# Kernel tuning notes

Measured on AMD Instinct MI355X. Metric: run time of the kernel, lower is better.

The kernel has to match this reference:

```python
import jax, jax.numpy as jnp
import numpy as np
from jax import lax

B, S = 4, 2048
HIDDEN = 1024
OUT = 1024
NUM_TABLE = 64
CODE_LEN = 10
TABLE_SIZE = 2 ** CODE_LEN  # 1024
TOTAL_DIM = NUM_TABLE * CODE_LEN  # 640


def setup_inputs() -> dict:
    key = jax.random.key(0)
    k1, k2, k3, k4, k5 = jax.random.split(key, 5)
    hidden_states = jax.random.normal(k1, (B, S, HIDDEN), dtype=jnp.float32)
    # nn.Linear(hidden_size, total_dim): weight [total_dim, hidden] in torch; store as [hidden, total_dim]
    W_proj = jax.random.normal(k2, (HIDDEN, TOTAL_DIM), dtype=jnp.float32) * (1.0 / np.sqrt(HIDDEN))
    b_proj = jax.random.normal(k3, (TOTAL_DIM,), dtype=jnp.float32) * 0.01
    tables = 0.02 * jax.random.normal(k4, (NUM_TABLE * TABLE_SIZE, OUT), dtype=jnp.float32)
    bias = 0.001 * jax.random.normal(k5, (OUT,), dtype=jnp.float32)
    return {"hidden_states": hidden_states, "W_proj": W_proj, "b_proj": b_proj,
            "tables": tables, "bias": bias}


def reference(hidden_states, W_proj, b_proj, tables, bias):
    other_shape = hidden_states.shape[:-1]
    x = hidden_states.reshape(-1, HIDDEN)  # [N, H], N = B*S
    # Hashing: dense projection then per-table code/score
    z = x @ W_proj + b_proj                       # [N, total_dim]
    z = z.reshape(-1, NUM_TABLE, CODE_LEN)        # [N, T, L]
    t = jnp.tanh(jnp.abs(z))
    score = jnp.prod((1.0 + t) * 0.5, axis=-1)    # [N, T] prob of selected bucket
    pow2 = (2 ** jnp.arange(CODE_LEN, dtype=jnp.int32))
    code = jnp.sum((z > 0).astype(jnp.int32) * pow2, axis=-1)  # [N, T] in [0, TABLE_SIZE)

    # Gather + weighted sum over tables, streamed with scan to avoid [N, T, OUT]
    tabs = tables.reshape(NUM_TABLE, TABLE_SIZE, OUT)
    code_t = code.T    # [T, N]
    score_t = score.T  # [T, N]

    def body(acc, inp):
        tab, idx, w = inp  # tab [TABLE_SIZE, OUT], idx [N], w [N]
        return acc + tab[idx] * w[:, None], None

    acc0 = jnp.zeros((x.shape[0], OUT), dtype=hidden_states.dtype)
    out, _ = lax.scan(body, acc0, (tabs, code_t, score_t))
    out = out + bias
    return out.reshape(*other_shape, OUT)
```

## Files before the change

### kernel.cpp

```cpp
#include <hip/hip_runtime.h>
#include <cstddef>
#include <cstdint>

#define HIDDEN    1024
#define OUTD      1024
#define NUM_TABLE 64
#define CODE_LEN  10
#define TABLE_SZ  1024
#define TOTAL_DIM 640

#define TAU   1e-3f
#define FCAP  131072u

typedef float  fx4    __attribute__((ext_vector_type(4)));
typedef ushort ux4    __attribute__((ext_vector_type(4)));
typedef ushort ux8    __attribute__((ext_vector_type(8)));
typedef short  bf16x8 __attribute__((ext_vector_type(8)));
typedef float  f32x4  __attribute__((ext_vector_type(4)));

struct bfp { ushort hi, lo; };
static __device__ __forceinline__ bfp split2(float v) {
    uint32_t u  = __float_as_uint(v);
    float    fh = __uint_as_float(u & 0xFFFF0000u);
    uint32_t ul = __float_as_uint(v - fh);
    bfp r; r.hi = (ushort)(u >> 16); r.lo = (ushort)(ul >> 16);
    return r;
}
static __device__ __forceinline__ ushort f2bf(float f) {
    uint32_t u = __float_as_uint(f);
    return (ushort)((u + 0x7FFFu + ((u >> 16) & 1u)) >> 16);
}

__global__ __launch_bounds__(256)
void split_wt(const float* __restrict__ W, ushort* __restrict__ wht,
              ushort* __restrict__ wlt, float* __restrict__ wt32)
{
    __shared__ float t[32][33];
    const int d0 = blockIdx.x * 32, k0 = blockIdx.y * 32;
    const int lx = threadIdx.x & 31, ly = threadIdx.x >> 5;
    #pragma unroll
    for (int i = 0; i < 32; i += 8)
        t[ly + i][lx] = W[(size_t)(k0 + ly + i) * TOTAL_DIM + d0 + lx];
    __syncthreads();
    #pragma unroll
    for (int i = 0; i < 32; i += 8) {
        float v = t[lx][ly + i];
        bfp s = split2(v);
        size_t o = (size_t)(d0 + ly + i) * HIDDEN + k0 + lx;
        wht[o] = s.hi; wlt[o] = s.lo; wt32[o] = v;
    }
}

#define GBM 64
#define GBN 64
#define GBK 32
#define LDK 40
#define GEMM_MB (8192 / GBM)
#define GEMM_NB (TOTAL_DIM / GBN)
#define GEMM_BLKS (GEMM_MB * GEMM_NB)
#define CONV_BLKS 1024

__global__ __launch_bounds__(256)
void gemm_convert(const float* __restrict__ x, const ushort* __restrict__ wht,
                  const ushort* __restrict__ wlt, const float* __restrict__ bproj,
                  float* __restrict__ z,
                  const float* __restrict__ tables, ushort* __restrict__ btab)
{
    __shared__ ushort Ah[GBM][LDK];
    __shared__ ushort Al[GBM][LDK];
    __shared__ ushort Bh[GBN][LDK];
    __shared__ ushort Bl[GBN][LDK];

    const int gb  = blockIdx.x;
    const int tid = threadIdx.x;

    if (gb >= GEMM_BLKS) {
        const int cb = gb - GEMM_BLKS;
        const int n4 = NUM_TABLE * TABLE_SZ * (OUTD / 4);
        const fx4* tp = (const fx4*)tables;
        const int stride = CONV_BLKS * 256;
        for (int i = cb * 256 + tid; i < n4; i += stride) {
            fx4 v = __builtin_nontemporal_load(&tp[i]);
            ux4 u;
            u.x = f2bf(v.x); u.y = f2bf(v.y); u.z = f2bf(v.z); u.w = f2bf(v.w);
            *(ux4*)&btab[(size_t)i * 4] = u;
        }
        return;
    }

    const int lane = tid & 63, wid = tid >> 6;
    const int wr = wid >> 1, wc = wid & 1;
    const int brow = (gb % GEMM_MB) * GBM;
    const int bcol = (gb / GEMM_MB) * GBN;
    const int fr = lane & 15, fq = lane >> 4;

    f32x4 acc[2][2] = {};

    for (int k0 = 0; k0 < HIDDEN; k0 += GBK) {
        #pragma unroll
        for (int i = 0; i < 2; ++i) {
            int c = tid + i * 256;
            int r = c >> 3, kc = (c & 7) * 4;
            fx4 v = *(const fx4*)&x[(size_t)(brow + r) * HIDDEN + k0 + kc];
            bfp s0 = split2(v.x), s1 = split2(v.y), s2 = split2(v.z), s3 = split2(v.w);
            ux4 h, l;
            h.x = s0.hi; l.x = s0.lo;
            h.y = s1.hi; l.y = s1.lo;
            h.z = s2.hi; l.z = s2.lo;
            h.w = s3.hi; l.w = s3.lo;
            *(ux4*)&Ah[r][kc] = h;
            *(ux4*)&Al[r][kc] = l;
        }
        {
            int nr = tid >> 2, kc = (tid & 3) * 8;
            size_t o = (size_t)(bcol + nr) * HIDDEN + k0 + kc;
            *(ux8*)&Bh[nr][kc] = *(const ux8*)&wht[o];
            *(ux8*)&Bl[nr][kc] = *(const ux8*)&wlt[o];
        }
        __syncthreads();

        bf16x8 ah[2], al[2], bh[2], bl[2];
        #pragma unroll
        for (int m = 0; m < 2; ++m) {
            ah[m] = *(const bf16x8*)&Ah[wr * 32 + m * 16 + fr][fq * 8];
            al[m] = *(const bf16x8*)&Al[wr * 32 + m * 16 + fr][fq * 8];
        }
        #pragma unroll
        for (int n = 0; n < 2; ++n) {
            bh[n] = *(const bf16x8*)&Bh[wc * 32 + n * 16 + fr][fq * 8];
            bl[n] = *(const bf16x8*)&Bl[wc * 32 + n * 16 + fr][fq * 8];
        }
        #pragma unroll
        for (int m = 0; m < 2; ++m)
            #pragma unroll
            for (int n = 0; n < 2; ++n) {
                acc[m][n] = __builtin_amdgcn_mfma_f32_16x16x32_bf16(ah[m], bh[n], acc[m][n], 0, 0, 0);
                acc[m][n] = __builtin_amdgcn_mfma_f32_16x16x32_bf16(ah[m], bl[n], acc[m][n], 0, 0, 0);
                acc[m][n] = __builtin_amdgcn_mfma_f32_16x16x32_bf16(al[m], bh[n], acc[m][n], 0, 0, 0);
            }
        __syncthreads();
    }

    #pragma unroll
    for (int n = 0; n < 2; ++n) {
        int col = bcol + wc * 32 + n * 16 + fr;
        float bb = bproj[col];
        #pragma unroll
        for (int m = 0; m < 2; ++m) {
            int rbase = brow + wr * 32 + m * 16 + fq * 4;
            #pragma unroll
            for (int j = 0; j < 4; ++j)
                z[(size_t)(rbase + j) * TOTAL_DIM + col] = acc[m][n][j] + bb;
        }
    }
}

__global__ __launch_bounds__(256)
void code_score2(const float* __restrict__ z, int* __restrict__ code,
                 float* __restrict__ score, uint32_t* __restrict__ flags,
                 uint32_t* __restrict__ cnt, int NT)
{
    int idx = blockIdx.x * 256 + threadIdx.x;
    bool live = idx < NT;
    int n = idx >> 6;
    int t = idx & 63;
    const int lane = threadIdx.x & 63;
    const float* zp = z + (size_t)n * TOTAL_DIM + t * CODE_LEN;
    float s = 1.0f;
    int   c = 0;
    #pragma unroll
    for (int i = 0; i < CODE_LEN; ++i) {
        float v = live ? zp[i] : 1.0f;
        bool  p = fabsf(v) < TAU;
        unsigned long long mask = __ballot(p);
        if (mask) {
            int nact = __popcll(mask);
            int lead = __ffsll((long long)mask) - 1;
            uint32_t base = 0;
            if (lane == lead) base = atomicAdd(cnt, (uint32_t)nact);
            base = (uint32_t)__shfl((int)base, lead);
            if (p) {
                uint32_t slot = base + (uint32_t)__popcll(mask & ((1ull << lane) - 1ull));
                if (slot < FCAP) {
                    uint32_t nd = (uint32_t)(n * TOTAL_DIM + t * CODE_LEN + i);
                    flags[slot] = nd | (v > 0.0f ? 0x80000000u : 0u);
                }
            }
        }
        s *= 0.5f * (1.0f + tanhf(fabsf(v)));
        c |= (v > 0.0f) ? (1 << i) : 0;
    }
    if (live) {
        code[idx]  = c;
        score[idx] = s;
    }
}

__global__ __launch_bounds__(256)
void fixz(const float* __restrict__ x, const float* __restrict__ wt32,
          const float* __restrict__ bproj, int* __restrict__ code,
          const uint32_t* __restrict__ flags, const uint32_t* __restrict__ cnt)
{
    const int lane = threadIdx.x & 63;
    const int gw   = (blockIdx.x * 256 + threadIdx.x) >> 6;
    const int nw   = (gridDim.x * 256) >> 6;
    uint32_t count = *cnt;
    if (count > FCAP) count = FCAP;

    for (uint32_t f = gw; f < count; f += nw) {
        uint32_t fl = flags[f];
        uint32_t e  = fl & 0x7FFFFFFFu;
        int oldpos  = (int)(fl >> 31);
        int n = e / TOTAL_DIM, d = e % TOTAL_DIM;
        const float* xr = x    + (size_t)n * HIDDEN;
        const float* wr = wt32 + (size_t)d * HIDDEN;
        float p = 0.0f;
        #pragma unroll
        for (int j = 0; j < 16; ++j) {
            int k = lane + j * 64;
            p = fmaf(xr[k], wr[k], p);
        }
        #pragma unroll
        for (int off = 32; off; off >>= 1) p += __shfl_xor(p, off);
        float v = p + bproj[d];
        if (lane == 0) {
            if ((v > 0.0f) != (oldpos != 0)) {
                int t = d / CODE_LEN, i = d % CODE_LEN;
                atomicXor(&code[n * NUM_TABLE + t], 1 << i);
            }
        }
    }
}

__global__ __launch_bounds__(256)
void gather_sum_bf16(const ushort* __restrict__ btab, const float* __restrict__ bias,
                     const int* __restrict__ code, const float* __restrict__ score,
                     float* __restrict__ out)
{
    __shared__ int   sc[NUM_TABLE];
    __shared__ float sw[NUM_TABLE];

    const int n   = blockIdx.x;
    const int tid = threadIdx.x;

    if (tid < NUM_TABLE) {
        sc[tid] = code[n * NUM_TABLE + tid];
        sw[tid] = score[n * NUM_TABLE + tid];
    }
    __syncthreads();

    float4 acc = *(const float4*)&bias[tid * 4];

    #pragma unroll 4
    for (int t = 0; t < NUM_TABLE; ++t) {
        const ux4 v = *(const ux4*)&btab[((size_t)(t * TABLE_SZ + sc[t])) * OUTD + tid * 4];
        float w = sw[t];
        acc.x += w * __uint_as_float((uint32_t)v.x << 16);
        acc.y += w * __uint_as_float((uint32_t)v.y << 16);
        acc.z += w * __uint_as_float((uint32_t)v.z << 16);
        acc.w += w * __uint_as_float((uint32_t)v.w << 16);
    }

    *(float4*)&out[(size_t)n * OUTD + tid * 4] = acc;
}

#define BM 64
#define BN 64
#define BK 32
__global__ __launch_bounds__(256)
void gemm_proj(const float* __restrict__ x, const float* __restrict__ W,
               const float* __restrict__ bproj, float* __restrict__ z)
{
    __shared__ float As[BK][BM + 4];
    __shared__ float Bs[BK][BN];
    const int tid  = threadIdx.x;
    const int brow = blockIdx.x * BM;
    const int bcol = blockIdx.y * BN;
    const int tr   = tid >> 4;
    const int tc   = tid & 15;
    float acc[4][4] = {};
    for (int k0 = 0; k0 < HIDDEN; k0 += BK) {
        #pragma unroll
        for (int i = 0; i < 2; ++i) {
            int lin = tid + i * 256;
            int r = lin >> 3, c8 = lin & 7;
            float4 a = *(const float4*)&x[(size_t)(brow + r) * HIDDEN + k0 + c8 * 4];
            As[c8 * 4 + 0][r] = a.x; As[c8 * 4 + 1][r] = a.y;
            As[c8 * 4 + 2][r] = a.z; As[c8 * 4 + 3][r] = a.w;
        }
        #pragma unroll
        for (int i = 0; i < 2; ++i) {
            int lin = tid + i * 256;
            int kk = lin >> 4, m4 = lin & 15;
            *(float4*)&Bs[kk][m4 * 4] =
                *(const float4*)&W[(size_t)(k0 + kk) * TOTAL_DIM + bcol + m4 * 4];
        }
        __syncthreads();
        #pragma unroll
        for (int kk = 0; kk < BK; ++kk) {
            float4 a = *(const float4*)&As[kk][tr * 4];
            float4 b = *(const float4*)&Bs[kk][tc * 4];
            acc[0][0] += a.x * b.x; acc[0][1] += a.x * b.y; acc[0][2] += a.x * b.z; acc[0][3] += a.x * b.w;
            acc[1][0] += a.y * b.x; acc[1][1] += a.y * b.y; acc[1][2] += a.y * b.z; acc[1][3] += a.y * b.w;
            acc[2][0] += a.z * b.x; acc[2][1] += a.z * b.y; acc[2][2] += a.z * b.z; acc[2][3] += a.z * b.w;
            acc[3][0] += a.w * b.x; acc[3][1] += a.w * b.y; acc[3][2] += a.w * b.z; acc[3][3] += a.w * b.w;
        }
        __syncthreads();
    }
    float4 bb = *(const float4*)&bproj[bcol + tc * 4];
    #pragma unroll
    for (int i = 0; i < 4; ++i) {
        int r = brow + tr * 4 + i;
        float4 o = {acc[i][0] + bb.x, acc[i][1] + bb.y, acc[i][2] + bb.z, acc[i][3] + bb.w};
        *(float4*)&z[(size_t)r * TOTAL_DIM + bcol + tc * 4] = o;
    }
}

__global__ __launch_bounds__(256)
void code_score(const float* __restrict__ z, int* __restrict__ code,
                float* __restrict__ score, int NT)
{
    int idx = blockIdx.x * 256 + threadIdx.x;
    if (idx >= NT) return;
    int n = idx >> 6, t = idx & 63;
    const float* zp = z + (size_t)n * TOTAL_DIM + t * CODE_LEN;
    float s = 1.0f; int c = 0;
    #pragma unroll
    for (int i = 0; i < CODE_LEN; ++i) {
        float v = zp[i];
        s *= 0.5f * (1.0f + tanhf(fabsf(v)));
        c |= (v > 0.0f) ? (1 << i) : 0;
    }
    code[idx] = c; score[idx] = s;
}

__global__ __launch_bounds__(256)
void gather_sum_f32(const float* __restrict__ tables, const float* __restrict__ bias,
                    const int* __restrict__ code, const float* __restrict__ score,
                    float* __restrict__ out)
{
    __shared__ int   sc[NUM_TABLE];
    __shared__ float sw[NUM_TABLE];
    const int n = blockIdx.x, tid = threadIdx.x;
    if (tid < NUM_TABLE) {
        sc[tid] = code[n * NUM_TABLE + tid];
        sw[tid] = score[n * NUM_TABLE + tid];
    }
    __syncthreads();
    float4 acc = *(const float4*)&bias[tid * 4];
    #pragma unroll 4
    for (int t = 0; t < NUM_TABLE; ++t) {
        const float* row = tables + ((size_t)(t * TABLE_SZ + sc[t])) * OUTD;
        float4 v = *(const float4*)&row[tid * 4];
        float w = sw[t];
        acc.x += v.x * w; acc.y += v.y * w; acc.z += v.z * w; acc.w += v.w * w;
    }
    *(float4*)&out[(size_t)n * OUTD + tid * 4] = acc;
}

extern "C" void kernel_launch(void* const* d_in, const int* in_sizes, int n_in,
                              void* d_out, int out_size, void* d_ws, size_t ws_size,
                              hipStream_t stream) {
    const float* x      = (const float*)d_in[0];
    const float* W      = (const float*)d_in[1];
    const float* bproj  = (const float*)d_in[2];
    const float* tables = (const float*)d_in[3];
    const float* bias   = (const float*)d_in[4];
    float* out = (float*)d_out;

    const int N = in_sizes[0] / HIDDEN;

    char* ws = (char*)d_ws;
    size_t off_z     = 0;
    size_t off_code  = off_z     + (size_t)N * TOTAL_DIM * sizeof(float);
    size_t off_score = off_code  + (size_t)N * NUM_TABLE * sizeof(int);
    size_t off_wht   = off_score + (size_t)N * NUM_TABLE * sizeof(float);
    size_t off_wlt   = off_wht   + (size_t)TOTAL_DIM * HIDDEN * sizeof(ushort);
    size_t off_wt32  = off_wlt   + (size_t)TOTAL_DIM * HIDDEN * sizeof(ushort);
    size_t off_flags = off_wt32  + (size_t)TOTAL_DIM * HIDDEN * sizeof(float);
    size_t off_cnt   = off_flags + (size_t)FCAP * sizeof(uint32_t);
    size_t off_btab  = (off_cnt + 4 + 255) & ~(size_t)255;
    size_t tab_elems = (size_t)NUM_TABLE * TABLE_SZ * OUTD;
    size_t need      = off_btab + tab_elems * sizeof(ushort);

    float*    z     = (float*)(ws + off_z);
    int*      code  = (int*)(ws + off_code);
    float*    score = (float*)(ws + off_score);
    ushort*   wht   = (ushort*)(ws + off_wht);
    ushort*   wlt   = (ushort*)(ws + off_wlt);
    float*    wt32  = (float*)(ws + off_wt32);
    uint32_t* flags = (uint32_t*)(ws + off_flags);
    uint32_t* cnt   = (uint32_t*)(ws + off_cnt);
    ushort*   btab  = (ushort*)(ws + off_btab);

    int NT = N * NUM_TABLE;

    if (ws_size >= need) {
        dim3 gw(TOTAL_DIM / 32, HIDDEN / 32);
        split_wt<<<gw, 256, 0, stream>>>(W, wht, wlt, wt32);
        (void)hipMemsetAsync(cnt, 0, 4, stream);

        gemm_convert<<<GEMM_BLKS + CONV_BLKS, 256, 0, stream>>>(
            x, wht, wlt, bproj, z, tables, btab);

        code_score2<<<(NT + 255) / 256, 256, 0, stream>>>(z, code, score, flags, cnt, NT);
        fixz<<<512, 256, 0, stream>>>(x, wt32, bproj, code, flags, cnt);

        gather_sum_bf16<<<N, 256, 0, stream>>>(btab, bias, code, score, out);
    } else {
        dim3 g1(N / BM, TOTAL_DIM / BN);
        gemm_proj<<<g1, 256, 0, stream>>>(x, W, bproj, z);
        code_score<<<(NT + 255) / 256, 256, 0, stream>>>(z, code, score, NT);
        gather_sum_f32<<<N, 256, 0, stream>>>(tables, bias, code, score, out);
    }
}
```

Baseline: 327.2 us.

## Regroup bf16 tables by 32-column slices and gather per column group

The fp32-to-bf16 table conversion now writes the tables in a column-grouped layout: 32 groups of 32 output columns, each group holding all tables and rows contiguously. The gather kernel is restructured so each block handles one column group for 64 tokens, with each thread loading 16-byte rows of its group. This keeps each block's working set to one column slice of the tables, about 4 MB, so it can stay cache-resident across tokens, instead of touching full 2 KB rows per token. The block index is mapped so neighbouring blocks share a column group. In exchange, the conversion writes are scattered, and each gather load is only 16 bytes per thread with lane groups reading separate rows.

Measured after the change: 325.2 us. Within noise of the previous version (-0.6%).

```diff
diff --git a/kernel.cpp b/kernel.cpp
--- a/kernel.cpp
+++ b/kernel.cpp
@@ -59,6 +59,8 @@
 #define GEMM_NB (TOTAL_DIM / GBN)
 #define GEMM_BLKS (GEMM_MB * GEMM_NB)
 #define CONV_BLKS 1024
+#define CPG 32
+#define NGRP (OUTD / CPG)
 
 __global__ __launch_bounds__(256)
 void gemm_convert(const float* __restrict__ x, const ushort* __restrict__ wht,
@@ -83,7 +85,13 @@
             fx4 v = __builtin_nontemporal_load(&tp[i]);
             ux4 u;
             u.x = f2bf(v.x); u.y = f2bf(v.y); u.z = f2bf(v.z); u.w = f2bf(v.w);
-            *(ux4*)&btab[(size_t)i * 4] = u;
+            int col4 = (i & 255) * 4;
+            int row  = (i >> 8) & 1023;
+            int t    = i >> 18;
+            int g    = col4 >> 5;
+            int c    = col4 & 31;
+            size_t o = ((((size_t)g * NUM_TABLE + t) * TABLE_SZ + row) << 5) + c;
+            *(ux4*)&btab[o] = u;
         }
         return;
     }
@@ -232,36 +240,54 @@
     }
 }
 
-__global__ __launch_bounds__(256)
-void gather_sum_bf16(const ushort* __restrict__ btab, const float* __restrict__ bias,
-                     const int* __restrict__ code, const float* __restrict__ score,
-                     float* __restrict__ out)
-{
-    __shared__ int   sc[NUM_TABLE];
-    __shared__ float sw[NUM_TABLE];
-
-    const int n   = blockIdx.x;
+#define TPB 64
+__global__ __launch_bounds__(256)
+void gather_grouped(const ushort* __restrict__ btab, const float* __restrict__ bias,
+                    const int* __restrict__ code, const float* __restrict__ score,
+                    float* __restrict__ out)
+{
+    __shared__ int   sc[TPB][NUM_TABLE + 1];
+    __shared__ float sw[TPB][NUM_TABLE + 1];
+
+    const int b   = blockIdx.x;
+    const int g   = (b & 7) + 8 * (b >> 10);
+    const int tch = (b >> 3) & 127;
+    const int n0  = tch * TPB;
     const int tid = threadIdx.x;
 
-    if (tid < NUM_TABLE) {
-        sc[tid] = code[n * NUM_TABLE + tid];
-        sw[tid] = score[n * NUM_TABLE + tid];
+    for (int i = tid; i < TPB * NUM_TABLE; i += 256) {
+        int tok = i >> 6, t = i & 63;
+        sc[tok][t] = __builtin_nontemporal_load(&code[(n0 + tok) * NUM_TABLE + t]);
+        sw[tok][t] = __builtin_nontemporal_load(&score[(n0 + tok) * NUM_TABLE + t]);
     }
     __syncthreads();
 
-    float4 acc = *(const float4*)&bias[tid * 4];
+    const int tok = tid >> 2;
+    const int sub = tid & 3;
+    const ushort* tbase = btab + (size_t)g * NUM_TABLE * TABLE_SZ * CPG;
+
+    float acc[8];
+    {
+        const float* bp = &bias[g * CPG + sub * 8];
+        #pragma unroll
+        for (int j = 0; j < 8; ++j) acc[j] = bp[j];
+    }
 
     #pragma unroll 4
     for (int t = 0; t < NUM_TABLE; ++t) {
-        const ux4 v = *(const ux4*)&btab[((size_t)(t * TABLE_SZ + sc[t])) * OUTD + tid * 4];
-        float w = sw[t];
-        acc.x += w * __uint_as_float((uint32_t)v.x << 16);
-        acc.y += w * __uint_as_float((uint32_t)v.y << 16);
-        acc.z += w * __uint_as_float((uint32_t)v.z << 16);
-        acc.w += w * __uint_as_float((uint32_t)v.w << 16);
-    }
-
-    *(float4*)&out[(size_t)n * OUTD + tid * 4] = acc;
+        int   c = sc[tok][t];
+        float w = sw[tok][t];
+        const ux8 v = *(const ux8*)&tbase[(((size_t)t * TABLE_SZ + c) << 5) + sub * 8];
+        #pragma unroll
+        for (int j = 0; j < 8; ++j)
+            acc[j] += w * __uint_as_float((uint32_t)v[j] << 16);
+    }
+
+    fx4 o0 = {acc[0], acc[1], acc[2], acc[3]};
+    fx4 o1 = {acc[4], acc[5], acc[6], acc[7]};
+    float* op = &out[(size_t)(n0 + tok) * OUTD + g * CPG + sub * 8];
+    __builtin_nontemporal_store(o0, (fx4*)op);
+    __builtin_nontemporal_store(o1, (fx4*)(op + 4));
 }
 
 #define BM 64
@@ -406,7 +432,7 @@
         code_score2<<<(NT + 255) / 256, 256, 0, stream>>>(z, code, score, flags, cnt, NT);
         fixz<<<512, 256, 0, stream>>>(x, wt32, bproj, code, flags, cnt);
 
-        gather_sum_bf16<<<N, 256, 0, stream>>>(btab, bias, code, score, out);
+        gather_grouped<<<NGRP * (N / TPB), 256, 0, stream>>>(btab, bias, code, score, out);
     } else {
         dim3 g1(N / BM, TOTAL_DIM / BN);
         gemm_proj<<<g1, 256, 0, stream>>>(x, W, bproj, z);
```
